# Kernel tuning notes

Hardware: AMD Instinct MI355X
Metric: run time of the kernel (lower is better)

Reference implementation:

```python
import jax, jax.numpy as jnp
import numpy as np
import math

B, S, H, NH, HD = 2, 2048, 4096, 32, 128  # batch, seq, hidden, heads, head_dim
ROPE_BASE = 10000.0


def setup_inputs() -> dict:
    key = jax.random.key(0)
    k1, k2 = jax.random.split(key)
    hidden_states = jax.random.normal(k1, (B, S, H), jnp.float32) * 0.02
    W_pack = jax.random.normal(k2, (3 * H, H), jnp.float32) * (1.0 / math.sqrt(H))
    position_ids = jnp.tile(jnp.arange(S, dtype=jnp.int64)[None, :], (B, 1))
    # 4D additive causal mask, as passed by HF Baichuan to this attention module
    causal = jnp.triu(jnp.full((S, S), -1e9, jnp.float32), 1)[None, None, :, :]
    return {"hidden_states": hidden_states, "W_pack": W_pack,
            "attention_mask": causal, "position_ids": position_ids}


def _rope(x, position_ids):
    # x: [B, S, NH, HD]; NeoX-style rotate-half RoPE over full head_dim
    half = HD // 2
    inv_freq = 1.0 / (ROPE_BASE ** (jnp.arange(half, dtype=jnp.float32) / half))
    ang = position_ids.astype(jnp.float32)[:, :, None] * inv_freq  # [B,S,half]
    cos = jnp.concatenate([jnp.cos(ang), jnp.cos(ang)], axis=-1)[:, :, None, :]
    sin = jnp.concatenate([jnp.sin(ang), jnp.sin(ang)], axis=-1)[:, :, None, :]
    x1, x2 = jnp.split(x, 2, axis=-1)
    x_rot = jnp.concatenate([-x2, x1], axis=-1)
    return x * cos + x_rot * sin


def reference(hidden_states, W_pack, attention_mask, position_ids):
    # fused QKV projection (W_pack has no bias in Baichuan)
    proj = hidden_states @ W_pack.T                      # [B,S,3H]
    q, k, v = jnp.split(proj, 3, axis=-1)
    q = q.reshape(B, S, NH, HD)
    k = k.reshape(B, S, NH, HD)
    v = v.reshape(B, S, NH, HD)
    q = _rope(q, position_ids)
    k = _rope(k, position_ids)
    # scaled dot-product attention
    scale = 1.0 / math.sqrt(HD)
    q = q.transpose(0, 2, 1, 3)  # [B,NH,S,HD]
    k = k.transpose(0, 2, 1, 3)
    v = v.transpose(0, 2, 1, 3)
    scores = jnp.einsum("bhqd,bhkd->bhqk", q, k) * scale + attention_mask
    probs = jax.nn.softmax(scores, axis=-1)
    ctx = jnp.einsum("bhqk,bhkd->bhqd", probs, v)        # [B,NH,S,HD]
    attn_output = ctx.transpose(0, 2, 1, 3).reshape(B, S, H)
    return attn_output
```

## Files before the change

### kernel.cpp

```cpp
#include <hip/hip_runtime.h>
#include <hip/hip_bf16.h>
#include <stdint.h>

typedef unsigned short u16;
typedef __attribute__((ext_vector_type(8))) short s16x8;
typedef __attribute__((ext_vector_type(8))) unsigned short u16x8;
typedef __attribute__((ext_vector_type(4))) unsigned short u16x4;
typedef __attribute__((ext_vector_type(4))) float fx4;
typedef __bf16 bf16x8 __attribute__((ext_vector_type(8)));

#define SEQ 2048
#define HID 4096
#define NHEAD 32
#define HDIM 128
#define P3H 12288
#define NKT 64

__device__ __forceinline__ u16 f2bf(float f) {
  unsigned u = __builtin_bit_cast(unsigned, f);
  u += 0x7fffu + ((u >> 16) & 1u);
  return (u16)(u >> 16);
}
__device__ __forceinline__ float bf2f(u16 h) {
  unsigned u = ((unsigned)h) << 16;
  return __builtin_bit_cast(float, u);
}
__device__ __forceinline__ void gload_lds16(const void* g, void* l) {
  __builtin_amdgcn_global_load_lds((const __attribute__((address_space(1))) void*)g,
                                   (__attribute__((address_space(3))) void*)l, 16, 0, 0);
}
__device__ __forceinline__ fx4 mfma16(s16x8 a, s16x8 b, fx4 c) {
  return __builtin_amdgcn_mfma_f32_16x16x32_bf16(
      __builtin_bit_cast(bf16x8, a), __builtin_bit_cast(bf16x8, b), c, 0, 0, 0);
}

__global__ void k_cvt2(const float* __restrict__ s0, u16* __restrict__ d0, int n0,
                       const float* __restrict__ s1, u16* __restrict__ d1, int n1) {
  int i = blockIdx.x * blockDim.x + threadIdx.x;
  const float* src; u16* dst;
  if (i < n0) { src = s0; dst = d0; }
  else        { src = s1; dst = d1; i -= n0; if (i >= n1) return; }
  float4 v = reinterpret_cast<const float4*>(src)[i];
  u16x4 o;
  o[0] = f2bf(v.x); o[1] = f2bf(v.y); o[2] = f2bf(v.z); o[3] = f2bf(v.w);
  reinterpret_cast<u16x4*>(dst)[i] = o;
}

__device__ __forceinline__ void stage_half(const u16* __restrict__ g, u16* l, int r0, int t) {
#pragma unroll
  for (int c = 0; c < 2; c++) {
    int row = r0 + c * 64 + (t >> 3);
    int blk = (t & 7) ^ ((t >> 3) & 7);
    gload_lds16(g + (size_t)row * HID + blk * 8, l + row * 64 + (t & 7) * 8);
  }
}

#define BAR_OPEN __builtin_amdgcn_s_barrier()
#define BAR_CLOSE do { __builtin_amdgcn_s_barrier(); __builtin_amdgcn_sched_barrier(0); } while (0)
#define LGKM0 do { asm volatile("s_waitcnt lgkmcnt(0)" ::: "memory"); \
                   __builtin_amdgcn_sched_barrier(0); } while (0)

#define LDA_QUAD(qm) do { \
  _Pragma("unroll") for (int mi = 0; mi < 4; mi++) \
  _Pragma("unroll") for (int ks = 0; ks < 2; ks++) { \
    int row = wrr + (qm) * 64 + mi * 16 + li; \
    aA[mi][ks] = *(const s16x8*)&Al[row * 64 + (((ks * 4 + lg) ^ (row & 7)) << 3)]; \
  } } while (0)

#define LDB_QUAD(qn) do { \
  _Pragma("unroll") for (int ni = 0; ni < 2; ni++) \
  _Pragma("unroll") for (int ks = 0; ks < 2; ks++) { \
    int row = wcc + (qn) * 32 + ni * 16 + li; \
    aB[qn][ni][ks] = *(const s16x8*)&Bl[row * 64 + (((ks * 4 + lg) ^ (row & 7)) << 3)]; \
  } } while (0)

#define MMA_QUAD(qm, qn) do { \
  _Pragma("unroll") for (int ks = 0; ks < 2; ks++) \
  _Pragma("unroll") for (int mi = 0; mi < 4; mi++) \
  _Pragma("unroll") for (int ni = 0; ni < 2; ni++) \
    acc[(qm) * 4 + mi][(qn) * 2 + ni] = \
        mfma16(aA[mi][ks], aB[qn][ni][ks], acc[(qm) * 4 + mi][(qn) * 2 + ni]); \
  } while (0)

__global__ void __launch_bounds__(512, 2) k_gemm_qkv(const u16* __restrict__ A,
                                                     const u16* __restrict__ W,
                                                     u16* __restrict__ C) {
  __shared__ u16 SM[2][2][256 * 64];
  const int t = threadIdx.x;
  const int lane = t & 63;
  const int w = t >> 6;
  const int li = lane & 15, lg = lane >> 4;
  const int wr = w >> 2, wc = w & 3;
  const int wrr = wr * 128, wcc = wc * 64;

  const int cpx = gridDim.x >> 3;
  const int swz = (blockIdx.x & 7) * cpx + (blockIdx.x >> 3);
  const int bm = swz / 48, bn = swz - bm * 48;
  const int m0 = bm * 256, n0 = bn * 256;

  const u16* Ag = A + (size_t)m0 * HID;
  const u16* Wg = W + (size_t)n0 * HID;

  fx4 acc[8][4];
#pragma unroll
  for (int i = 0; i < 8; i++)
#pragma unroll
    for (int j = 0; j < 4; j++) acc[i][j] = fx4{0.f, 0.f, 0.f, 0.f};
  s16x8 aA[4][2], aB[2][2][2];

  stage_half(Wg, &SM[0][1][0], 0, t);
  stage_half(Wg, &SM[0][1][0], 128, t);
  stage_half(Ag, &SM[0][0][0], 0, t);
  stage_half(Ag, &SM[0][0][0], 128, t);
  stage_half(Wg + 64, &SM[1][1][0], 0, t);
  stage_half(Wg + 64, &SM[1][1][0], 128, t);
  asm volatile("s_waitcnt vmcnt(4)" ::: "memory");
  BAR_CLOSE;

  for (int kt = 0; kt < NKT; kt++) {
    const int cur = kt & 1;
    u16* Al = &SM[cur][0][0];
    u16* Bl = &SM[cur][1][0];
    u16* Anxt = &SM[cur ^ 1][0][0];
    const u16* Agn = Ag + (size_t)(kt + 1) * 64;
    const u16* Wgn = Wg + (size_t)(kt + 2) * 64;

    LDA_QUAD(0);
    LDB_QUAD(0);
    if (kt + 1 < NKT) stage_half(Agn, Anxt, 0, t);
    asm volatile("s_waitcnt lgkmcnt(8)" ::: "memory");
    BAR_OPEN;
    LGKM0;
    __builtin_amdgcn_s_setprio(1);
    MMA_QUAD(0, 0);
    __builtin_amdgcn_s_setprio(0);
    BAR_CLOSE;

    LDB_QUAD(1);
    if (kt + 1 < NKT) stage_half(Agn, Anxt, 128, t);
    BAR_OPEN;
    LGKM0;
    __builtin_amdgcn_s_setprio(1);
    MMA_QUAD(0, 1);
    __builtin_amdgcn_s_setprio(0);
    BAR_CLOSE;

    LDA_QUAD(1);
    if (kt + 2 < NKT) stage_half(Wgn, Bl, 0, t);
    BAR_OPEN;
    LGKM0;
    __builtin_amdgcn_s_setprio(1);
    MMA_QUAD(1, 1);
    __builtin_amdgcn_s_setprio(0);
    BAR_CLOSE;

    if (kt + 2 < NKT) stage_half(Wgn, Bl, 128, t);
    BAR_OPEN;
    LGKM0;
    __builtin_amdgcn_s_setprio(1);
    MMA_QUAD(1, 0);
    __builtin_amdgcn_s_setprio(0);
    if (kt + 2 < NKT) {
      asm volatile("s_waitcnt vmcnt(4)" ::: "memory");
    } else {
      asm volatile("s_waitcnt vmcnt(0)" ::: "memory");
    }
    BAR_CLOSE;
  }

#pragma unroll
  for (int mi = 0; mi < 8; mi++)
#pragma unroll
    for (int ni = 0; ni < 4; ni++)
#pragma unroll
      for (int j = 0; j < 4; j++) {
        int r = m0 + wrr + mi * 16 + lg * 4 + j;
        int c = n0 + wcc + ni * 16 + li;
        C[(size_t)r * P3H + c] = f2bf(acc[mi][ni][j]);
      }
}

__global__ void k_rope(const u16* __restrict__ proj, u16* __restrict__ q,
                       u16* __restrict__ k, const int* __restrict__ pos_ids) {
  int t = blockIdx.x * 256 + threadIdx.x;
  int d = t & 63;
  int h = (t >> 6) & 31;
  int s = (t >> 11) & 2047;
  int b = t >> 22;
  int prow = b * SEQ + s;
  const u16* pr = proj + (size_t)prow * P3H;
  float q1 = bf2f(pr[h * HDIM + d]);
  float q2 = bf2f(pr[h * HDIM + d + 64]);
  float k1 = bf2f(pr[HID + h * HDIM + d]);
  float k2 = bf2f(pr[HID + h * HDIM + d + 64]);
  float p = (float)pos_ids[prow];
  float invf = exp2f(-(float)d * 0.2076205059304601f);
  float ang = p * invf;
  float sn, cs;
  sincosf(ang, &sn, &cs);
  size_t base = ((size_t)(b * NHEAD + h) * SEQ + s) * HDIM + d;
  q[base]      = f2bf(q1 * cs - q2 * sn);
  q[base + 64] = f2bf(q2 * cs + q1 * sn);
  k[base]      = f2bf(k1 * cs - k2 * sn);
  k[base + 64] = f2bf(k2 * cs + k1 * sn);
}

__global__ void k_vtrans(const u16* __restrict__ proj, u16* __restrict__ vt) {
  int wid = (blockIdx.x * 256 + threadIdx.x) >> 6;
  int lane = threadIdx.x & 63;
  int half = wid & 1;
  int s8 = (wid >> 1) & 255;
  int h = (wid >> 9) & 31;
  int b = wid >> 14;
  int d = half * 64 + lane;
  int s0 = s8 * 8;
  u16x8 v;
#pragma unroll
  for (int r = 0; r < 8; r++)
    v[r] = proj[(size_t)(b * SEQ + s0 + r) * P3H + 2 * HID + h * HDIM + d];
  *reinterpret_cast<u16x8*>(&vt[((size_t)(b * NHEAD + h) * HDIM + d) * SEQ + s0]) = v;
}

__device__ __forceinline__ void stage_kv(const u16* __restrict__ kp, const u16* __restrict__ vp,
                                         u16* ksl, u16* vsl, int kv0, int t) {
#pragma unroll
  for (int c = 0; c < 4; c++) {
    int row = c * 16 + (t >> 4);
    int cb = (t & 15) ^ (row & 7);
    gload_lds16(kp + (size_t)(kv0 + row) * HDIM + cb * 8, ksl + (size_t)(c * 256 + t) * 8);
  }
#pragma unroll
  for (int c = 0; c < 4; c++) {
    int row = c * 32 + (t >> 3);
    int cb = (t & 7) ^ (row & 7);
    gload_lds16(vp + (size_t)row * SEQ + kv0 + cb * 8, vsl + (size_t)(c * 256 + t) * 8);
  }
}

__global__ void __launch_bounds__(256, 2) k_attn(const u16* __restrict__ q,
                                                 const u16* __restrict__ k,
                                                 const u16* __restrict__ vt,
                                                 float* __restrict__ out) {
  __shared__ u16 Ks[2][64 * 128];
  __shared__ u16 Vs[2][128 * 64];
  __shared__ u16 Ps[4][2][16 * 64];
  const int t = threadIdx.x;
  const int w = t >> 6, lane = t & 63;
  const int li = lane & 15, lg = lane >> 4;
  const int bh = blockIdx.x;
  const int qb = gridDim.y - 1 - blockIdx.y;
  const int b = bh >> 5, h = bh & 31;
  const int qw = qb * 128 + w * 32;
  const u16* qp = q + (size_t)bh * SEQ * HDIM;
  const u16* kp = k + (size_t)bh * SEQ * HDIM;
  const u16* vp = vt + (size_t)bh * HDIM * SEQ;

  s16x8 bq[2][4];
#pragma unroll
  for (int g = 0; g < 2; g++)
#pragma unroll
    for (int kk = 0; kk < 4; kk++)
      bq[g][kk] = *reinterpret_cast<const s16x8*>(
          &qp[(size_t)(qw + g * 16 + li) * HDIM + kk * 32 + lg * 8]);

  fx4 Oacc[2][8];
#pragma unroll
  for (int g = 0; g < 2; g++)
#pragma unroll
    for (int nd = 0; nd < 8; nd++) Oacc[g][nd] = fx4{0.f, 0.f, 0.f, 0.f};
  float mrun[2] = {-1e30f, -1e30f}, lrun[2] = {0.f, 0.f};

  const float SC2 = 0.12752551286084110f;
  const float THR = 8.0f / SC2;
  const int nt = 2 * (qb + 1);
  const int psw = (li & 7) << 4;

  stage_kv(kp, vp, Ks[0], Vs[0], 0, t);

  for (int tk = 0; tk < nt; tk++) {
    const int cur = tk & 1;
    if (tk + 1 < nt) {
      stage_kv(kp, vp, Ks[cur ^ 1], Vs[cur ^ 1], (tk + 1) * 64, t);
      asm volatile("s_waitcnt vmcnt(8)" ::: "memory");
    } else {
      asm volatile("s_waitcnt vmcnt(0)" ::: "memory");
    }
    __builtin_amdgcn_s_barrier();

    const u16* Kc = Ks[cur];
    const u16* Vc = Vs[cur];
    const int kv0 = tk * 64;
    const bool diag = (tk >= 2 * qb);

    fx4 sc[2][4];
#pragma unroll
    for (int g = 0; g < 2; g++)
#pragma unroll
      for (int n = 0; n < 4; n++) sc[g][n] = fx4{0.f, 0.f, 0.f, 0.f};
    __builtin_amdgcn_s_setprio(1);
#pragma unroll
    for (int n = 0; n < 4; n++) {
      int r = n * 16 + li;
#pragma unroll
      for (int kk = 0; kk < 4; kk++) {
        s16x8 ak = *reinterpret_cast<const s16x8*>(
            &Kc[r * 128 + (((kk * 4 + lg) ^ (r & 7)) << 3)]);
        sc[0][n] = mfma16(ak, bq[0][kk], sc[0][n]);
        sc[1][n] = mfma16(ak, bq[1][kk], sc[1][n]);
      }
    }
    __builtin_amdgcn_s_setprio(0);

    if (diag) {
#pragma unroll
      for (int g = 0; g < 2; g++) {
        const int qg = qw + g * 16 + li;
#pragma unroll
        for (int n = 0; n < 4; n++)
#pragma unroll
          for (int j = 0; j < 4; j++) {
            int kvg = kv0 + n * 16 + lg * 4 + j;
            if (kvg > qg) sc[g][n][j] = -1e30f;
          }
      }
    }

    s16x8 ap[2][2];
#pragma unroll
    for (int g = 0; g < 2; g++) {
      float mn[4];
#pragma unroll
      for (int n = 0; n < 4; n++)
        mn[n] = fmaxf(fmaxf(sc[g][n][0], sc[g][n][1]), fmaxf(sc[g][n][2], sc[g][n][3]));
      float vmax = fmaxf(fmaxf(mn[0], mn[1]), fmaxf(mn[2], mn[3]));
      vmax = fmaxf(vmax, __shfl_xor(vmax, 16));
      vmax = fmaxf(vmax, __shfl_xor(vmax, 32));
      if (__any(vmax > mrun[g] + THR)) {
        float mnew = fmaxf(mrun[g], vmax);
        float al = exp2f((mrun[g] - mnew) * SC2);
        mrun[g] = mnew;
        lrun[g] *= al;
        float alj[4];
#pragma unroll
        for (int j = 0; j < 4; j++) alj[j] = __shfl(al, lg * 4 + j);
#pragma unroll
        for (int nd = 0; nd < 8; nd++)
#pragma unroll
          for (int j = 0; j < 4; j++) Oacc[g][nd][j] *= alj[j];
      }
      const float mS = mrun[g] * SC2;
      float ps[4];
#pragma unroll
      for (int n = 0; n < 4; n++) {
        u16x4 pk;
        float pv0 = exp2f(__builtin_fmaf(sc[g][n][0], SC2, -mS));
        float pv1 = exp2f(__builtin_fmaf(sc[g][n][1], SC2, -mS));
        float pv2 = exp2f(__builtin_fmaf(sc[g][n][2], SC2, -mS));
        float pv3 = exp2f(__builtin_fmaf(sc[g][n][3], SC2, -mS));
        pk[0] = __builtin_bit_cast(u16, __float2bfloat16(pv0));
        pk[1] = __builtin_bit_cast(u16, __float2bfloat16(pv1));
        pk[2] = __builtin_bit_cast(u16, __float2bfloat16(pv2));
        pk[3] = __builtin_bit_cast(u16, __float2bfloat16(pv3));
        ps[n] = (pv0 + pv1) + (pv2 + pv3);
        *reinterpret_cast<u16x4*>(
            &Ps[w][g][li * 64 + (((n * 32 + lg * 8) ^ psw) >> 1)]) = pk;
      }
      float psum = (ps[0] + ps[1]) + (ps[2] + ps[3]);
      psum += __shfl_xor(psum, 16);
      psum += __shfl_xor(psum, 32);
      lrun[g] += psum;
#pragma unroll
      for (int kvc = 0; kvc < 2; kvc++)
        ap[g][kvc] = *reinterpret_cast<const s16x8*>(
            &Ps[w][g][li * 64 + (((kvc * 64 + lg * 16) ^ psw) >> 1)]);
    }

    __builtin_amdgcn_s_setprio(1);
#pragma unroll
    for (int nd = 0; nd < 8; nd++) {
      int dr = nd * 16 + li;
#pragma unroll
      for (int kvc = 0; kvc < 2; kvc++) {
        s16x8 bv = *reinterpret_cast<const s16x8*>(
            &Vc[dr * 64 + (((kvc * 4 + lg) ^ (dr & 7)) << 3)]);
        Oacc[0][nd] = mfma16(ap[0][kvc], bv, Oacc[0][nd]);
        Oacc[1][nd] = mfma16(ap[1][kvc], bv, Oacc[1][nd]);
      }
    }
    __builtin_amdgcn_s_setprio(0);

    __builtin_amdgcn_s_barrier();
    __builtin_amdgcn_sched_barrier(0);
  }

#pragma unroll
  for (int g = 0; g < 2; g++)
#pragma unroll
    for (int j = 0; j < 4; j++) {
      float rl = 1.0f / __shfl(lrun[g], lg * 4 + j);
      int s = qw + g * 16 + lg * 4 + j;
      float* op = out + ((size_t)(b * SEQ) + s) * HID + h * HDIM;
#pragma unroll
      for (int nd = 0; nd < 8; nd++) op[nd * 16 + li] = Oacc[g][nd][j] * rl;
    }
}

extern "C" void kernel_launch(void* const* d_in, const int* in_sizes, int n_in,
                              void* d_out, int out_size, void* d_ws, size_t ws_size,
                              hipStream_t stream) {
  const float* hidden = (const float*)d_in[0];
  const float* wpack = (const float*)d_in[1];
  const int* pos = (const int*)d_in[3];
  float* out = (float*)d_out;

  char* ws = (char*)d_ws;
  u16* hid_bf = (u16*)ws;
  u16* wp_bf = (u16*)(ws + ((size_t)32 << 20));
  u16* qb = (u16*)ws;
  u16* kb = (u16*)(ws + ((size_t)32 << 20));
  u16* vtb = (u16*)(ws + ((size_t)64 << 20));
  u16* proj = (u16*)(ws + ((size_t)128 << 20));

  const int n4h = HID * HID / 4, n4w = P3H * HID / 4;
  k_cvt2<<<(n4h + n4w + 255) / 256, 256, 0, stream>>>(hidden, hid_bf, n4h, wpack, wp_bf, n4w);

  k_gemm_qkv<<<768, 512, 0, stream>>>(hid_bf, wp_bf, proj);

  k_rope<<<(2 * SEQ * NHEAD * 64) / 256, 256, 0, stream>>>(proj, qb, kb, pos);
  k_vtrans<<<(2 * NHEAD * (SEQ / 8) * 2) / 4, 256, 0, stream>>>(proj, vtb);

  dim3 ga(2 * NHEAD, SEQ / 128);
  k_attn<<<ga, 256, 0, stream>>>(qb, kb, vtb, out);
}
```

Before: 560.5 us.

## Fuse RoPE and V transpose into the QKV GEMM epilogue via LDS staging

```diff
diff --git a/kernel.cpp b/kernel.cpp
--- a/kernel.cpp
+++ b/kernel.cpp
@@ -82,9 +82,14 @@
         mfma16(aA[mi][ks], aB[qn][ni][ks], acc[(qm) * 4 + mi][(qn) * 2 + ni]); \
   } while (0)
 
+#define LTIDX(c, r) (((c) << 8) + ((r) ^ (((c) & 31) << 3)))
+
 __global__ void __launch_bounds__(512, 2) k_gemm_qkv(const u16* __restrict__ A,
                                                      const u16* __restrict__ W,
-                                                     u16* __restrict__ C) {
+                                                     u16* __restrict__ qo,
+                                                     u16* __restrict__ ko,
+                                                     u16* __restrict__ vo,
+                                                     const int* __restrict__ pos) {
   __shared__ u16 SM[2][2][256 * 64];
   const int t = threadIdx.x;
   const int lane = t & 63;
@@ -168,57 +173,53 @@
     BAR_CLOSE;
   }
 
+  u16* LT = &SM[0][0][0];
+
 #pragma unroll
   for (int mi = 0; mi < 8; mi++)
 #pragma unroll
-    for (int ni = 0; ni < 4; ni++)
-#pragma unroll
-      for (int j = 0; j < 4; j++) {
-        int r = m0 + wrr + mi * 16 + lg * 4 + j;
-        int c = n0 + wcc + ni * 16 + li;
-        C[(size_t)r * P3H + c] = f2bf(acc[mi][ni][j]);
-      }
-}
-
-__global__ void k_rope(const u16* __restrict__ proj, u16* __restrict__ q,
-                       u16* __restrict__ k, const int* __restrict__ pos_ids) {
-  int t = blockIdx.x * 256 + threadIdx.x;
-  int d = t & 63;
-  int h = (t >> 6) & 31;
-  int s = (t >> 11) & 2047;
-  int b = t >> 22;
-  int prow = b * SEQ + s;
-  const u16* pr = proj + (size_t)prow * P3H;
-  float q1 = bf2f(pr[h * HDIM + d]);
-  float q2 = bf2f(pr[h * HDIM + d + 64]);
-  float k1 = bf2f(pr[HID + h * HDIM + d]);
-  float k2 = bf2f(pr[HID + h * HDIM + d + 64]);
-  float p = (float)pos_ids[prow];
-  float invf = exp2f(-(float)d * 0.2076205059304601f);
-  float ang = p * invf;
-  float sn, cs;
-  sincosf(ang, &sn, &cs);
-  size_t base = ((size_t)(b * NHEAD + h) * SEQ + s) * HDIM + d;
-  q[base]      = f2bf(q1 * cs - q2 * sn);
-  q[base + 64] = f2bf(q2 * cs + q1 * sn);
-  k[base]      = f2bf(k1 * cs - k2 * sn);
-  k[base + 64] = f2bf(k2 * cs + k1 * sn);
-}
-
-__global__ void k_vtrans(const u16* __restrict__ proj, u16* __restrict__ vt) {
-  int wid = (blockIdx.x * 256 + threadIdx.x) >> 6;
-  int lane = threadIdx.x & 63;
-  int half = wid & 1;
-  int s8 = (wid >> 1) & 255;
-  int h = (wid >> 9) & 31;
-  int b = wid >> 14;
-  int d = half * 64 + lane;
-  int s0 = s8 * 8;
-  u16x8 v;
-#pragma unroll
-  for (int r = 0; r < 8; r++)
-    v[r] = proj[(size_t)(b * SEQ + s0 + r) * P3H + 2 * HID + h * HDIM + d];
-  *reinterpret_cast<u16x8*>(&vt[((size_t)(b * NHEAD + h) * HDIM + d) * SEQ + s0]) = v;
+    for (int ni = 0; ni < 4; ni++) {
+      u16x4 pk;
+#pragma unroll
+      for (int j = 0; j < 4; j++) pk[j] = f2bf(acc[mi][ni][j]);
+      int c = wcc + ni * 16 + li;
+      int r0 = wrr + mi * 16 + lg * 4;
+      *reinterpret_cast<u16x4*>(&LT[LTIDX(c, r0)]) = pk;
+    }
+  __syncthreads();
+
+  const int ttype = n0 >> 12;
+  const int h0 = (n0 & 4095) >> 7;
+  const int bb = m0 >> 11;
+  const int sB = m0 & 2047;
+
+  if (ttype < 2) {
+    u16* dst = (ttype == 0) ? qo : ko;
+    const float LG2E4 = 0.2076205059304601f;
+    float invf = exp2f(-(float)lane * LG2E4);
+    for (int it = 0; it < 64; ++it) {
+      int i = w * 64 + it;
+      int hh = i & 1, r = i >> 1;
+      float x1 = bf2f(LT[LTIDX(hh * 128 + lane, r)]);
+      float x2 = bf2f(LT[LTIDX(hh * 128 + lane + 64, r)]);
+      float p = (float)pos[m0 + r];
+      float sn, cs;
+      sincosf(p * invf, &sn, &cs);
+      size_t base = ((size_t)(bb * NHEAD + h0 + hh) * SEQ + sB + r) * HDIM;
+      dst[base + lane]      = f2bf(x1 * cs - x2 * sn);
+      dst[base + lane + 64] = f2bf(x2 * cs + x1 * sn);
+    }
+  } else {
+    for (int it = 0; it < 16; ++it) {
+      int cp = w * 16 + it;
+      int c = cp * 2 + (lane >> 5);
+      int ch = lane & 31;
+      u16x8 v = *reinterpret_cast<const u16x8*>(&LT[LTIDX(c, ch * 8)]);
+      int hh = c >> 7, d = c & 127;
+      size_t base = ((size_t)(bb * NHEAD + h0 + hh) * HDIM + d) * SEQ + sB;
+      *reinterpret_cast<u16x8*>(&vo[base + ch * 8]) = v;
+    }
+  }
 }
 
 __device__ __forceinline__ void stage_kv(const u16* __restrict__ kp, const u16* __restrict__ vp,
@@ -416,18 +417,14 @@
   char* ws = (char*)d_ws;
   u16* hid_bf = (u16*)ws;
   u16* wp_bf = (u16*)(ws + ((size_t)32 << 20));
-  u16* qb = (u16*)ws;
-  u16* kb = (u16*)(ws + ((size_t)32 << 20));
-  u16* vtb = (u16*)(ws + ((size_t)64 << 20));
-  u16* proj = (u16*)(ws + ((size_t)128 << 20));
+  u16* qb = (u16*)(ws + ((size_t)128 << 20));
+  u16* kb = (u16*)(ws + ((size_t)160 << 20));
+  u16* vtb = (u16*)(ws + ((size_t)192 << 20));
 
   const int n4h = HID * HID / 4, n4w = P3H * HID / 4;
   k_cvt2<<<(n4h + n4w + 255) / 256, 256, 0, stream>>>(hidden, hid_bf, n4h, wpack, wp_bf, n4w);
 
-  k_gemm_qkv<<<768, 512, 0, stream>>>(hid_bf, wp_bf, proj);
-
-  k_rope<<<(2 * SEQ * NHEAD * 64) / 256, 256, 0, stream>>>(proj, qb, kb, pos);
-  k_vtrans<<<(2 * NHEAD * (SEQ / 8) * 2) / 4, 256, 0, stream>>>(proj, vtb);
+  k_gemm_qkv<<<768, 512, 0, stream>>>(hid_bf, wp_bf, qb, kb, vtb, pos);
 
   dim3 ga(2 * NHEAD, SEQ / 128);
   k_attn<<<ga, 256, 0, stream>>>(qb, kb, vtb, out);
```

Result: faster. 544.1 us (-2.9%).
